# Kernel optimization log

Hardware: AMD Instinct MI355X
Metric: run time of the kernel (lower is better)

## Reference

```python
import jax, jax.numpy as jnp
import numpy as np
from jax import lax

B, S, E, H = 8, 1024, 1024, 16
HEAD_DIM = E // H
THRESHOLD = 0.5
NEG_FILL = -1e9


def setup_inputs() -> dict:
    key = jax.random.key(0)
    k0, k1, k2 = jax.random.split(key, 3)
    x = jax.random.normal(k0, (B, S, E), jnp.float32)
    in_proj_w = jax.random.normal(k1, (3 * E, E), jnp.float32) * 0.02
    in_proj_b = jnp.zeros((3 * E,), jnp.float32)
    out_proj_w = jax.random.normal(k2, (E, E), jnp.float32) * 0.02
    out_proj_b = jnp.zeros((E,), jnp.float32)
    return {"x": x, "in_proj_w": in_proj_w, "in_proj_b": in_proj_b,
            "out_proj_w": out_proj_w, "out_proj_b": out_proj_b}


def _mha(x, in_proj_w, in_proj_b, out_proj_w, out_proj_b):
    # PyTorch nn.MultiheadAttention with q=k=v=x, batch_first=True
    qkv = x @ in_proj_w.T + in_proj_b                     # [B,S,3E]
    q, k, v = jnp.split(qkv, 3, axis=-1)                  # each [B,S,E]
    def split_heads(t):
        return t.reshape(B, S, H, HEAD_DIM).transpose(0, 2, 1, 3)  # [B,H,S,d]
    q, k, v = split_heads(q), split_heads(k), split_heads(v)
    scale = 1.0 / np.sqrt(HEAD_DIM).astype(np.float32)
    scores = jnp.einsum('bhqd,bhkd->bhqk', q, k) * scale  # [B,H,S,S]
    w = jax.nn.softmax(scores, axis=-1)
    o = jnp.einsum('bhqk,bhkd->bhqd', w, v)               # [B,H,S,d]
    o = o.transpose(0, 2, 1, 3).reshape(B, S, E)
    attn_output = o @ out_proj_w.T + out_proj_b           # [B,S,E]
    attn_weights = w.mean(axis=1)                         # head-averaged [B,S,S]
    return attn_output, attn_weights


def _cluster(attn_weights):
    # Sequential greedy clustering: scan rows i in order; if row i is not yet
    # visited, its high-attention columns (> THRESHOLD) form cluster i and are
    # marked visited. cluster_id[b, j] = row index of the first cluster that
    # claimed token j, or -1 if never claimed.
    visited0 = jnp.zeros((B, S), dtype=bool)
    cid0 = jnp.full((B, S), -1, dtype=jnp.int32)

    def step(carry, i):
        visited, cid = carry
        process = ~jnp.take(visited, i, axis=1)           # [B] row i unvisited?
        high = jnp.take(attn_weights, i, axis=1) > THRESHOLD  # [B,S]
        claimed = process[:, None] & high                 # [B,S]
        newly = claimed & (~visited)
        cid = jnp.where(newly, jnp.int32(i), cid)
        visited = visited | claimed
        return (visited, cid), None

    (visited, cid), _ = lax.scan(step, (visited0, cid0), jnp.arange(S))
    return cid, visited


def reference(x, in_proj_w, in_proj_b, out_proj_w, out_proj_b):
    attn_output, attn_weights = _mha(x, in_proj_w, in_proj_b, out_proj_w, out_proj_b)
    cluster_ids, covered = _cluster(attn_weights)
    # _generate_image_features: x where token belongs to some cluster, -1e9 else
    clustered_outputs = jnp.where(covered[..., None], x, jnp.float32(NEG_FILL))
    return attn_output, attn_weights, clustered_outputs, cluster_ids
```

## Files before the change

### kernel.cpp

```cpp
#include <hip/hip_runtime.h>
#include <hip/hip_bf16.h>

#define B 8
#define S 1024
#define E 1024
#define H 16

typedef unsigned short u16;
typedef unsigned char u8;
typedef unsigned int u32;
typedef unsigned long long u64;

typedef __attribute__((ext_vector_type(8))) short s16x8;
typedef __attribute__((ext_vector_type(4))) float f32x4;
typedef __attribute__((ext_vector_type(16))) float f32x16;

__device__ __forceinline__ u16 f2bf(float f) {
    union { float f; u32 i; } x; x.f = f;
    u32 r = x.i + 0x7FFFu + ((x.i >> 16) & 1u);
    return (u16)(r >> 16);
}
__device__ __forceinline__ f32x16 zero16() {
    f32x16 z;
#pragma unroll
    for (int i = 0; i < 16; ++i) z[i] = 0.f;
    return z;
}
__device__ __forceinline__ void gload16(const u16* g, u16* l) {
    __builtin_amdgcn_global_load_lds(
        (const __attribute__((address_space(1))) u32*)g,
        (__attribute__((address_space(3))) u32*)l, 16, 0, 0);
}

__global__ __launch_bounds__(256) void cvt_all(
    const float* __restrict__ x, const float* __restrict__ w0,
    const float* __restrict__ w1, u16* __restrict__ xb,
    u16* __restrict__ wb0, u16* __restrict__ wb1) {
    int i = blockIdx.x * 256 + threadIdx.x;
    const float* src;
    u16* dst;
    int off;
    if (i < 2097152) { src = x; dst = xb; off = i; }
    else if (i < 2883584) { src = w0; dst = wb0; off = i - 2097152; }
    else { src = w1; dst = wb1; off = i - 2883584; }
    float4 v = ((const float4*)src)[off];
    union { u16 u[4]; ushort4 s; } p;
    p.u[0] = f2bf(v.x); p.u[1] = f2bf(v.y);
    p.u[2] = f2bf(v.z); p.u[3] = f2bf(v.w);
    ((ushort4*)dst)[off] = p.s;
}

__global__ __launch_bounds__(256) void gemm_qkv(
    const u16* __restrict__ A, const u16* __restrict__ W,
    const float* __restrict__ bias, u16* __restrict__ qb, u16* __restrict__ kb,
    u16* __restrict__ vt) {
    __shared__ __align__(16) u16 smem[16384];
    u16* As = smem;
    u16* Bs = smem + 8192;
    const int t = threadIdx.x;
    const int lane = t & 63;
    const int w = t >> 6;
    const int lin = (int)(blockIdx.y * gridDim.x + blockIdx.x);
    const int xcd = lin & 7;
    const int idx = lin >> 3;
    const int mt = (xcd & 3) * 16 + idx / 12;
    const int nt = (xcd >> 2) * 12 + idx % 12;
    const int m0 = mt * 128;
    const int n0 = nt * 128;
    const int wm = w >> 1, wn = w & 1;
    const int l15 = lane & 15, l4 = lane >> 4;
    const int lr = lane >> 3;
    const int lc = ((lane & 7) ^ lr) * 8;

    f32x4 acc[4][4];
#pragma unroll
    for (int i = 0; i < 4; ++i)
#pragma unroll
        for (int j = 0; j < 4; ++j) acc[i][j] = {0.f, 0.f, 0.f, 0.f};

    for (int k0 = 0; k0 < 1024; k0 += 64) {
        __syncthreads();
#pragma unroll
        for (int jj = 0; jj < 4; ++jj) {
            int j = w * 4 + jj;
            gload16(A + (size_t)(m0 + j * 8 + lr) * 1024 + k0 + lc, As + j * 512);
            gload16(W + (size_t)(n0 + j * 8 + lr) * 1024 + k0 + lc, Bs + j * 512);
        }
        __syncthreads();
#pragma unroll
        for (int ks = 0; ks < 2; ++ks) {
            s16x8 af[4], bf[4];
#pragma unroll
            for (int i = 0; i < 4; ++i) {
                int row = wm * 64 + i * 16 + l15;
                af[i] = *(const s16x8*)((const u8*)As +
                        (((row << 7) + (ks << 6) + (l4 << 4)) ^ ((row & 7) << 4)));
            }
#pragma unroll
            for (int j = 0; j < 4; ++j) {
                int row = wn * 64 + j * 16 + l15;
                bf[j] = *(const s16x8*)((const u8*)Bs +
                        (((row << 7) + (ks << 6) + (l4 << 4)) ^ ((row & 7) << 4)));
            }
#pragma unroll
            for (int i = 0; i < 4; ++i)
#pragma unroll
                for (int j = 0; j < 4; ++j)
                    acc[i][j] = __builtin_amdgcn_mfma_f32_16x16x32_bf16(
                        af[i], bf[j], acc[i][j], 0, 0, 0);
        }
    }

    __syncthreads();
    u16* Cs = smem;
    const int seg = n0 >> 10;
    const int bb = m0 >> 10;
    const int ms = m0 & 1023;
    if (seg < 2) {
        const float sc = (seg == 0) ? 0.18033688011f : 1.0f;
#pragma unroll
        for (int j = 0; j < 4; ++j) {
            int nl = wn * 64 + j * 16 + l15;
            float bn = bias[n0 + nl];
#pragma unroll
            for (int i = 0; i < 4; ++i) {
                int ml = wm * 64 + i * 16 + l4 * 4;
#pragma unroll
                for (int rr = 0; rr < 4; ++rr)
                    Cs[(ml + rr) * 128 + nl] = f2bf((acc[i][j][rr] + bn) * sc);
            }
        }
        __syncthreads();
        u16* dst0 = (seg == 0) ? qb : kb;
#pragma unroll
        for (int it = 0; it < 8; ++it) {
            int flat = it * 256 + t;
            int ml = flat >> 4;
            int g = (flat >> 3) & 1;
            int c8 = flat & 7;
            int hh = ((n0 + g * 64) & 1023) >> 6;
            u16* dst = dst0 + (((size_t)(bb * 16 + hh) * 1024 + ms + ml) << 6) + c8 * 8;
            *(uint4*)dst = *(const uint4*)(Cs + ml * 128 + g * 64 + c8 * 8);
        }
    } else {
#pragma unroll
        for (int j = 0; j < 4; ++j) {
            int nl = wn * 64 + j * 16 + l15;
            float bn = bias[n0 + nl];
            int sz = (nl & 7) << 4;
#pragma unroll
            for (int i = 0; i < 4; ++i) {
                int ml = wm * 64 + i * 16 + l4 * 4;
#pragma unroll
                for (int rr = 0; rr < 4; ++rr) {
                    int bl = (ml + rr) << 1;
                    *(u16*)((u8*)Cs + (nl << 8) + (bl ^ sz)) =
                        f2bf(acc[i][j][rr] + bn);
                }
            }
        }
        __syncthreads();
#pragma unroll
        for (int it = 0; it < 8; ++it) {
            int flat = it * 256 + t;
            int nl = flat >> 4;
            int c = flat & 15;
            int n = n0 + nl;
            int hh = (n & 1023) >> 6;
            int d = n & 63;
            u16* dst = vt + ((size_t)(bb * 16 + hh) * 64 + d) * 1024 + ms + c * 8;
            *(uint4*)dst = *(const uint4*)((u8*)Cs + (nl << 8) +
                                           ((c << 4) ^ ((nl & 7) << 4)));
        }
    }
}

__device__ __forceinline__ void gemm1_body(
    int lin, u16* smem, const u16* __restrict__ A, const u16* __restrict__ W,
    const float* __restrict__ bias, float* __restrict__ outf) {
    u16* As = smem;
    u16* Bs = smem + 8192;
    const int t = threadIdx.x;
    const int lane = t & 63;
    const int w = t >> 6;
    const int xcd = lin & 7;
    const int idx = lin >> 3;
    const int m0 = (xcd * 8 + idx / 8) * 128;
    const int n0 = (idx % 8) * 128;
    const int wm = w >> 1, wn = w & 1;
    const int l15 = lane & 15, l4 = lane >> 4;
    const int lr = lane >> 3;
    const int lc = ((lane & 7) ^ lr) * 8;

    f32x4 acc[4][4];
#pragma unroll
    for (int i = 0; i < 4; ++i)
#pragma unroll
        for (int j = 0; j < 4; ++j) acc[i][j] = {0.f, 0.f, 0.f, 0.f};

    for (int k0 = 0; k0 < 1024; k0 += 64) {
        __syncthreads();
#pragma unroll
        for (int jj = 0; jj < 4; ++jj) {
            int j = w * 4 + jj;
            gload16(A + (size_t)(m0 + j * 8 + lr) * 1024 + k0 + lc, As + j * 512);
            gload16(W + (size_t)(n0 + j * 8 + lr) * 1024 + k0 + lc, Bs + j * 512);
        }
        __syncthreads();
#pragma unroll
        for (int ks = 0; ks < 2; ++ks) {
            s16x8 af[4], bf[4];
#pragma unroll
            for (int i = 0; i < 4; ++i) {
                int row = wm * 64 + i * 16 + l15;
                af[i] = *(const s16x8*)((const u8*)As +
                        (((row << 7) + (ks << 6) + (l4 << 4)) ^ ((row & 7) << 4)));
            }
#pragma unroll
            for (int j = 0; j < 4; ++j) {
                int row = wn * 64 + j * 16 + l15;
                bf[j] = *(const s16x8*)((const u8*)Bs +
                        (((row << 7) + (ks << 6) + (l4 << 4)) ^ ((row & 7) << 4)));
            }
#pragma unroll
            for (int i = 0; i < 4; ++i)
#pragma unroll
                for (int j = 0; j < 4; ++j)
                    acc[i][j] = __builtin_amdgcn_mfma_f32_16x16x32_bf16(
                        af[i], bf[j], acc[i][j], 0, 0, 0);
        }
    }

    __syncthreads();
    float* Csf = (float*)smem;
#pragma unroll
    for (int r = 0; r < 2; ++r) {
        if (wm == r) {
#pragma unroll
            for (int j = 0; j < 4; ++j) {
                int nl = wn * 64 + j * 16 + l15;
                float bn = bias[n0 + nl];
#pragma unroll
                for (int i = 0; i < 4; ++i) {
                    int mlr = i * 16 + l4 * 4;
#pragma unroll
                    for (int rr = 0; rr < 4; ++rr)
                        Csf[(mlr + rr) * 128 + nl] = acc[i][j][rr] + bn;
                }
            }
        }
        __syncthreads();
#pragma unroll
        for (int it = 0; it < 8; ++it) {
            int flat = it * 256 + t;
            int row = flat >> 5;
            int c4 = flat & 31;
            *(float4*)(outf + (size_t)(m0 + r * 64 + row) * 1024 + n0 + c4 * 4) =
                *(const float4*)(Csf + row * 128 + c4 * 4);
        }
        __syncthreads();
    }
}

template <int BASE>
__device__ __forceinline__ s16x8 build_pa(f32x16 e) {
    u32 a, bv, c, d;
    asm("v_cvt_pk_bf16_f32 %0, %1, %2" : "=v"(a) : "v"(e[BASE + 0]), "v"(e[BASE + 1]));
    asm("v_cvt_pk_bf16_f32 %0, %1, %2" : "=v"(bv) : "v"(e[BASE + 2]), "v"(e[BASE + 3]));
    asm("v_cvt_pk_bf16_f32 %0, %1, %2" : "=v"(c) : "v"(e[BASE + 4]), "v"(e[BASE + 5]));
    asm("v_cvt_pk_bf16_f32 %0, %1, %2" : "=v"(d) : "v"(e[BASE + 6]), "v"(e[BASE + 7]));
    asm("v_permlane32_swap_b32 %0, %1" : "+v"(a), "+v"(c));
    asm("v_permlane32_swap_b32 %0, %1" : "+v"(bv), "+v"(d));
    union { u32 w[4]; s16x8 v; } u;
    u.w[0] = a; u.w[1] = bv; u.w[2] = c; u.w[3] = d;
    return u.v;
}
__device__ __forceinline__ float pair_sum(float v) {
    float a_ = v, b_ = v;
    asm("v_permlane32_swap_b32 %0, %1" : "+v"(a_), "+v"(b_));
    return a_ + b_;
}
__device__ __forceinline__ u32 pair_or(u32 v) {
    u32 a_ = v, b_ = v;
    asm("v_permlane32_swap_b32 %0, %1" : "+v"(a_), "+v"(b_));
    return a_ | b_;
}

__global__ __launch_bounds__(256, 3) void attn_flash(
    const u16* __restrict__ qg, const u16* __restrict__ kg,
    const u16* __restrict__ vtg, u16* __restrict__ og,
    float* __restrict__ stats) {
    __shared__ __align__(16) u16 bufK[2][64 * 64];
    __shared__ __align__(16) u16 bufV[2][64 * 64];
    const int t = threadIdx.x;
    const int lane = t & 63;
    const int w = t >> 6;
    const int task = ((blockIdx.x & 7) << 7) | (blockIdx.x >> 3);
    const int b = task >> 7;
    const int h = (task >> 3) & 15;
    const int qg_ = task & 7;
    const int q = lane & 31;
    const int hi = lane >> 5;
    const int q0 = qg_ * 128 + w * 32;
    const size_t hb = (size_t)(b * 16 + h) << 16;

    const int lr = lane >> 3;
    const int lc = ((lane & 7) ^ lr) * 8;
    const int swz = (q & 7) << 4;

#define STAGE(tt, bb)                                                          \
    do {                                                                       \
        _Pragma("unroll") for (int jj = 0; jj < 2; ++jj) {                     \
            int j = w * 2 + jj;                                                \
            gload16(kg + hb + (size_t)((tt) * 64 + j * 8 + lr) * 64 + lc,      \
                    bufK[bb] + j * 512);                                       \
            gload16(vtg + hb + (size_t)(j * 8 + lr) * 1024 + (tt) * 64 + lc,   \
                    bufV[bb] + j * 512);                                       \
        }                                                                      \
    } while (0)

    s16x8 qf[4];
#pragma unroll
    for (int s = 0; s < 4; ++s)
        qf[s] = *(const s16x8*)(qg + hb + (size_t)(q0 + q) * 64 + s * 16 + hi * 8);

    f32x16 oLo = zero16(), oHi = zero16();
    float l = 0.f;

    STAGE(0, 0);
    __syncthreads();
    int cur = 0;

    for (int tile = 0; tile < 16; ++tile) {
        if (tile < 15) STAGE(tile + 1, cur ^ 1);
        const u16* bK = bufK[cur];
        const u16* bV = bufV[cur];
        s16x8 ka0[4], ka1[4];
#pragma unroll
        for (int s = 0; s < 4; ++s) {
            ka0[s] = *(const s16x8*)((const u8*)bK +
                     (((q << 7) + (s << 5) + (hi << 4)) ^ swz));
            ka1[s] = *(const s16x8*)((const u8*)bK +
                     ((((32 + q) << 7) + (s << 5) + (hi << 4)) ^ swz));
        }
        f32x16 s0_ = zero16(), s1_ = zero16();
#pragma unroll
        for (int s = 0; s < 4; ++s) {
            s0_ = __builtin_amdgcn_mfma_f32_32x32x16_bf16(ka0[s], qf[s], s0_, 0, 0, 0);
            s1_ = __builtin_amdgcn_mfma_f32_32x32x16_bf16(ka1[s], qf[s], s1_, 0, 0, 0);
        }
        float t0 = 0.f, t1 = 0.f, t2 = 0.f, t3 = 0.f;
#pragma unroll
        for (int i = 0; i < 16; i += 4) {
            s0_[i + 0] = exp2f(s0_[i + 0]); s1_[i + 0] = exp2f(s1_[i + 0]);
            s0_[i + 1] = exp2f(s0_[i + 1]); s1_[i + 1] = exp2f(s1_[i + 1]);
            s0_[i + 2] = exp2f(s0_[i + 2]); s1_[i + 2] = exp2f(s1_[i + 2]);
            s0_[i + 3] = exp2f(s0_[i + 3]); s1_[i + 3] = exp2f(s1_[i + 3]);
            t0 += s0_[i + 0] + s1_[i + 0]; t1 += s0_[i + 1] + s1_[i + 1];
            t2 += s0_[i + 2] + s1_[i + 2]; t3 += s0_[i + 3] + s1_[i + 3];
        }
        l += pair_sum((t0 + t1) + (t2 + t3));
        s16x8 p00 = build_pa<0>(s0_), p01 = build_pa<8>(s0_);
        s16x8 p10 = build_pa<0>(s1_), p11 = build_pa<8>(s1_);
        s16x8 vA = *(const s16x8*)((const u8*)bV + (((q << 7) + 0 + (hi << 4)) ^ swz));
        s16x8 vB = *(const s16x8*)((const u8*)bV + ((((q + 32) << 7) + 0 + (hi << 4)) ^ swz));
        oLo = __builtin_amdgcn_mfma_f32_32x32x16_bf16(vA, p00, oLo, 0, 0, 0);
        oHi = __builtin_amdgcn_mfma_f32_32x32x16_bf16(vB, p00, oHi, 0, 0, 0);
        vA = *(const s16x8*)((const u8*)bV + (((q << 7) + 32 + (hi << 4)) ^ swz));
        vB = *(const s16x8*)((const u8*)bV + ((((q + 32) << 7) + 32 + (hi << 4)) ^ swz));
        oLo = __builtin_amdgcn_mfma_f32_32x32x16_bf16(vA, p01, oLo, 0, 0, 0);
        oHi = __builtin_amdgcn_mfma_f32_32x32x16_bf16(vB, p01, oHi, 0, 0, 0);
        vA = *(const s16x8*)((const u8*)bV + (((q << 7) + 64 + (hi << 4)) ^ swz));
        vB = *(const s16x8*)((const u8*)bV + ((((q + 32) << 7) + 64 + (hi << 4)) ^ swz));
        oLo = __builtin_amdgcn_mfma_f32_32x32x16_bf16(vA, p10, oLo, 0, 0, 0);
        oHi = __builtin_amdgcn_mfma_f32_32x32x16_bf16(vB, p10, oHi, 0, 0, 0);
        vA = *(const s16x8*)((const u8*)bV + (((q << 7) + 96 + (hi << 4)) ^ swz));
        vB = *(const s16x8*)((const u8*)bV + ((((q + 32) << 7) + 96 + (hi << 4)) ^ swz));
        oLo = __builtin_amdgcn_mfma_f32_32x32x16_bf16(vA, p11, oLo, 0, 0, 0);
        oHi = __builtin_amdgcn_mfma_f32_32x32x16_bf16(vB, p11, oHi, 0, 0, 0);
        __syncthreads();
        cur ^= 1;
    }
#undef STAGE
    float inv = 1.0f / l;
    oLo = oLo * inv;
    oHi = oHi * inv;
    u16* orow = og + (size_t)(b * 1024 + q0 + q) * 1024 + h * 64;
#pragma unroll
    for (int rg = 0; rg < 4; ++rg) {
        union { u16 u[4]; u64 v; } pk;
#pragma unroll
        for (int j = 0; j < 4; ++j) pk.u[j] = f2bf(oLo[4 * rg + j]);
        *(u64*)(orow + 8 * rg + 4 * hi) = pk.v;
#pragma unroll
        for (int j = 0; j < 4; ++j) pk.u[j] = f2bf(oHi[4 * rg + j]);
        *(u64*)(orow + 32 + 4 * hi + 8 * rg) = pk.v;
    }
    if (hi == 0)
        stats[(size_t)(b * 16 + h) * 1024 + q0 + q] = 4.0f + log2f(l);
}

__device__ __forceinline__ void aw_body(
    int bid, u16* smem, const u16* __restrict__ qg, const u16* __restrict__ kg,
    const float* __restrict__ stats, float* __restrict__ aw,
    u64* __restrict__ maskg) {
    u16* bufK = smem;
    u16* bufQ = smem + 8192;
    const int t = threadIdx.x;
    const int lane = t & 63;
    const int w = t >> 6;
    const int sw = ((bid & 7) << 7) | (bid >> 3);
    const int b = sw >> 7;
    const int ks = (sw >> 3) & 15;
    const int qg_ = sw & 7;
    const int q = lane & 31;
    const int hi = lane >> 5;
    const int q0 = qg_ * 128;
    const int qr = w * 32 + q;
    const int kbase = ks * 64;

    const int lr = lane >> 3;
    const int lc = ((lane & 7) ^ lr) * 8;
    const int swz = (q & 7) << 4;

#define STAGEAW(hh, bb)                                                        \
    do {                                                                       \
        const size_t hbs = (size_t)(b * 16 + (hh)) << 16;                      \
        _Pragma("unroll") for (int jj = 0; jj < 2; ++jj) {                     \
            int j = w * 2 + jj;                                                \
            gload16(kg + hbs + (size_t)(kbase + j * 8 + lr) * 64 + lc,         \
                    bufK + (bb) * 4096 + j * 512);                             \
        }                                                                      \
        _Pragma("unroll") for (int jj = 0; jj < 4; ++jj) {                     \
            int j = w * 4 + jj;                                                \
            gload16(qg + hbs + (size_t)(q0 + j * 8 + lr) * 64 + lc,            \
                    bufQ + (bb) * 8192 + j * 512);                             \
        }                                                                      \
    } while (0)

    f32x16 awA = zero16(), awB = zero16();

    STAGEAW(0, 0);
    __syncthreads();
    int cur = 0;

    for (int h = 0; h < 16; ++h) {
        if (h < 15) STAGEAW(h + 1, cur ^ 1);
        const u16* bK = bufK + cur * 4096;
        const u16* bQ = bufQ + cur * 8192;
        s16x8 qf[4], kA[4], kB[4];
#pragma unroll
        for (int s = 0; s < 4; ++s) {
            qf[s] = *(const s16x8*)((const u8*)bQ +
                    (((qr << 7) + (s << 5) + (hi << 4)) ^ swz));
            kA[s] = *(const s16x8*)((const u8*)bK +
                    (((q << 7) + (s << 5) + (hi << 4)) ^ swz));
            kB[s] = *(const s16x8*)((const u8*)bK +
                    ((((q + 32) << 7) + (s << 5) + (hi << 4)) ^ swz));
        }
        float C = stats[(size_t)(b * 16 + h) * 1024 + q0 + qr];
        f32x16 sA, sB;
        const float negC = -C;
#pragma unroll
        for (int i = 0; i < 16; ++i) { sA[i] = negC; sB[i] = negC; }
#pragma unroll
        for (int s = 0; s < 4; ++s) {
            sA = __builtin_amdgcn_mfma_f32_32x32x16_bf16(kA[s], qf[s], sA, 0, 0, 0);
            sB = __builtin_amdgcn_mfma_f32_32x32x16_bf16(kB[s], qf[s], sB, 0, 0, 0);
        }
#pragma unroll
        for (int i = 0; i < 16; ++i) {
            awA[i] += exp2f(sA[i]);
            awB[i] += exp2f(sB[i]);
        }
        __syncthreads();
        cur ^= 1;
    }
#undef STAGEAW
    float* awrow = aw + (size_t)(b * 1024 + q0 + qr) * 1024 + kbase;
#pragma unroll
    for (int rg = 0; rg < 4; ++rg) {
        *(float4*)(awrow + 8 * rg + 4 * hi) =
            make_float4(awA[4 * rg + 0], awA[4 * rg + 1], awA[4 * rg + 2], awA[4 * rg + 3]);
        *(float4*)(awrow + 32 + 8 * rg + 4 * hi) =
            make_float4(awB[4 * rg + 0], awB[4 * rg + 1], awB[4 * rg + 2], awB[4 * rg + 3]);
    }
    u32 lo = 0, hi32 = 0;
#pragma unroll
    for (int r = 0; r < 16; ++r) {
        int k = (r & 3) + 8 * (r >> 2) + 4 * hi;
        lo |= (awA[r] > 0.5f) ? (1u << k) : 0u;
        hi32 |= (awB[r] > 0.5f) ? (1u << k) : 0u;
    }
    lo = pair_or(lo);
    hi32 = pair_or(hi32);
    if (hi == 0)
        maskg[(size_t)(b * 1024 + q0 + qr) * 16 + ks] = ((u64)hi32 << 32) | (u64)lo;
}

__global__ __launch_bounds__(256, 3) void attn_aw_k(
    const u16* __restrict__ qg, const u16* __restrict__ kg,
    const float* __restrict__ stats, float* __restrict__ aw,
    u64* __restrict__ maskg) {
    __shared__ __align__(16) u16 sm[24576];
    aw_body((int)blockIdx.x, sm, qg, kg, stats, aw, maskg);
}
__global__ __launch_bounds__(256, 3) void gemm1_k(
    const u16* __restrict__ A, const u16* __restrict__ W,
    const float* __restrict__ bias, float* __restrict__ outf) {
    __shared__ __align__(16) u16 sm[16384];
    gemm1_body((int)blockIdx.x, sm, A, W, bias, outf);
}
__global__ __launch_bounds__(256, 3) void fused_aw_gemm1(
    const u16* __restrict__ qg, const u16* __restrict__ kg,
    const float* __restrict__ stats, float* __restrict__ aw,
    u64* __restrict__ maskg, const u16* __restrict__ o,
    const u16* __restrict__ w1, const float* __restrict__ bias,
    float* __restrict__ outf) {
    __shared__ __align__(16) u16 sm[24576];
    if (blockIdx.x < 1024)
        aw_body((int)blockIdx.x, sm, qg, kg, stats, aw, maskg);
    else
        gemm1_body((int)blockIdx.x - 1024, sm, o, w1, bias, outf);
}

__global__ __launch_bounds__(256) void cluster_kernel(
    const u64* __restrict__ maskg, float* __restrict__ cid, u64* __restrict__ cov) {
    __shared__ u64 mask[16384];
    __shared__ u16 rows[1024];
    const int t = threadIdx.x;
    const int b = blockIdx.x;
#pragma unroll
    for (int i = 0; i < 64; ++i)
        mask[t + 256 * i] = maskg[(size_t)b * 16384 + t + 256 * i];
#pragma unroll
    for (int i = 0; i < 4; ++i) cid[b * S + t + 256 * i] = -1.0f;
    __syncthreads();
    if (t < 64) {
        int nr = 0;
        for (int it = 0; it < 16; ++it) {
            int row = it * 64 + t;
            const u64* mp = mask + row * 16;
            u64 orv = 0;
#pragma unroll
            for (int j = 0; j < 16; ++j) orv |= mp[j];
            u64 bal = __ballot(orv != 0ULL);
            int pre = __popcll(bal & ((1ULL << t) - 1ULL));
            if (orv != 0ULL) rows[nr + pre] = (u16)row;
            nr += __popcll(bal);
        }
        u64 vis = 0;
        for (int idx = 0; idx < nr; ++idx) {
            int i = rows[idx];
            u64 viw = __shfl(vis, i >> 6);
            bool proc = ((viw >> (i & 63)) & 1ULL) == 0ULL;
            u64 cl = (proc && t < 16) ? mask[i * 16 + t] : 0ULL;
            u64 newly = cl & ~vis;
            vis |= cl;
            while (newly) {
                int bit = __ffsll((long long)newly) - 1;
                cid[b * S + t * 64 + bit] = (float)i;
                newly &= newly - 1;
            }
        }
        if (t < 16) cov[b * 16 + t] = vis;
    }
}

__global__ __launch_bounds__(256) void clustered_kernel(
    const float* __restrict__ x, const u64* __restrict__ cov,
    float* __restrict__ out2) {
    const size_t n4 = (size_t)B * S * E / 4;
    size_t idx = (size_t)blockIdx.x * 256 + threadIdx.x;
    const float4 neg = make_float4(-1e9f, -1e9f, -1e9f, -1e9f);
    for (; idx < n4; idx += (size_t)gridDim.x * 256) {
        size_t tok = idx >> 8;
        int bb = (int)(tok >> 10), s = (int)(tok & 1023);
        u64 m = cov[bb * 16 + (s >> 6)];
        bool c = ((m >> (s & 63)) & 1ULL) != 0ULL;
        float4 v = ((const float4*)x)[idx];
        ((float4*)out2)[idx] = c ? v : neg;
    }
}

extern "C" void kernel_launch(void* const* d_in, const int* in_sizes, int n_in,
                              void* d_out, int out_size, void* d_ws, size_t ws_size,
                              hipStream_t stream) {
    const float* x = (const float*)d_in[0];
    const float* w_in = (const float*)d_in[1];
    const float* b_in = (const float*)d_in[2];
    const float* w_out = (const float*)d_in[3];
    const float* b_out = (const float*)d_in[4];

    float* out0 = (float*)d_out;
    float* out1 = out0 + 8388608;
    float* out2 = out1 + 8388608;
    float* out3 = out2 + 8388608;

    if (ws_size >= ((size_t)37 << 20)) {
        u16* o_bf = (u16*)d_ws;
        u16* q_bf = (u16*)((char*)d_ws + ((size_t)16 << 20));
        u16* wb1 = (u16*)((char*)d_ws + ((size_t)32 << 20));
        float* statsF = (float*)((char*)d_ws + ((size_t)34 << 20));
        u64* maskg = (u64*)((char*)d_ws + ((size_t)34 << 20) + (1u << 19));
        u64* cov = (u64*)((char*)d_ws + ((size_t)35 << 20) + (1u << 19));
        u16* vt_bf = (u16*)out0;
        u16* xb = (u16*)out1;
        u16* wb0 = xb + 8388608;
        u16* k_bf = (u16*)out2;

        cvt_all<<<12288, 256, 0, stream>>>(x, w_in, w_out, xb, wb0, wb1);
        gemm_qkv<<<dim3(64, 24), 256, 0, stream>>>(xb, wb0, b_in, q_bf, k_bf, vt_bf);
        attn_flash<<<1024, 256, 0, stream>>>(q_bf, k_bf, vt_bf, o_bf, statsF);
        fused_aw_gemm1<<<1536, 256, 0, stream>>>(q_bf, k_bf, statsF, out1, maskg,
                                                 o_bf, wb1, b_out, out0);
        cluster_kernel<<<8, 256, 0, stream>>>(maskg, out3, cov);
        clustered_kernel<<<2048, 256, 0, stream>>>(x, cov, out2);
    } else {
        u16* q_bf = (u16*)out0;
        u16* vt_bf = q_bf + 8388608;
        u16* xb = (u16*)out1;
        u16* k_bf = (u16*)out2;
        u16* wb0 = k_bf + 8388608;
        u16* wb1 = wb0 + 3145728;
        float* statsF = (float*)(k_bf + 12582912);
        u16* o_bf = (u16*)d_ws;
        u64* maskg = (u64*)((char*)d_ws + (size_t)(16u << 20));
        u64* cov = (u64*)((char*)d_ws + (size_t)(17u << 20));

        cvt_all<<<12288, 256, 0, stream>>>(x, w_in, w_out, xb, wb0, wb1);
        gemm_qkv<<<dim3(64, 24), 256, 0, stream>>>(xb, wb0, b_in, q_bf, k_bf, vt_bf);
        attn_flash<<<1024, 256, 0, stream>>>(q_bf, k_bf, vt_bf, o_bf, statsF);
        attn_aw_k<<<1024, 256, 0, stream>>>(q_bf, k_bf, statsF, out1, maskg);
        gemm1_k<<<512, 256, 0, stream>>>(o_bf, wb1, b_out, out0);
        cluster_kernel<<<8, 256, 0, stream>>>(maskg, out3, cov);
        clustered_kernel<<<2048, 256, 0, stream>>>(x, cov, out2);
    }
}
```

Before: 222.2 us.

## Rewrite QKV GEMM with 256x256 tiles and a multi-stage async-load pipeline

Recasts the QKV projection GEMM as 512-thread blocks that each compute a 256x256 output tile from a 128KB shared buffer. K-tiles are prefetched two stages ahead in quadrant pieces, with vmcnt-based waits, raw barriers and setprio around the MFMA bursts. The goal is to overlap global loads with matrix math and to cut how often A and W are reloaded from memory. In exchange, shared memory per block and register pressure rise, and only 384 blocks are launched.

```diff
diff --git a/kernel.cpp b/kernel.cpp
--- a/kernel.cpp
+++ b/kernel.cpp
@@ -50,66 +50,97 @@
     ((ushort4*)dst)[off] = p.s;
 }
 
-__global__ __launch_bounds__(256) void gemm_qkv(
+__global__ __launch_bounds__(512, 2) void gemm_qkv(
     const u16* __restrict__ A, const u16* __restrict__ W,
     const float* __restrict__ bias, u16* __restrict__ qb, u16* __restrict__ kb,
     u16* __restrict__ vt) {
-    __shared__ __align__(16) u16 smem[16384];
-    u16* As = smem;
-    u16* Bs = smem + 8192;
+    __shared__ __align__(16) u16 smem[65536];
     const int t = threadIdx.x;
     const int lane = t & 63;
     const int w = t >> 6;
-    const int lin = (int)(blockIdx.y * gridDim.x + blockIdx.x);
+    const int lin = (int)blockIdx.x;
     const int xcd = lin & 7;
     const int idx = lin >> 3;
-    const int mt = (xcd & 3) * 16 + idx / 12;
-    const int nt = (xcd >> 2) * 12 + idx % 12;
-    const int m0 = mt * 128;
-    const int n0 = nt * 128;
-    const int wm = w >> 1, wn = w & 1;
+    const int mt = (xcd & 3) * 8 + idx / 6;
+    const int nt = (xcd >> 2) * 6 + idx % 6;
+    const int m0 = mt * 256;
+    const int n0 = nt * 256;
     const int l15 = lane & 15, l4 = lane >> 4;
     const int lr = lane >> 3;
     const int lc = ((lane & 7) ^ lr) * 8;
-
-    f32x4 acc[4][4];
-#pragma unroll
-    for (int i = 0; i < 4; ++i)
-#pragma unroll
-        for (int j = 0; j < 4; ++j) acc[i][j] = {0.f, 0.f, 0.f, 0.f};
-
-    for (int k0 = 0; k0 < 1024; k0 += 64) {
-        __syncthreads();
-#pragma unroll
-        for (int jj = 0; jj < 4; ++jj) {
-            int j = w * 4 + jj;
-            gload16(A + (size_t)(m0 + j * 8 + lr) * 1024 + k0 + lc, As + j * 512);
-            gload16(W + (size_t)(n0 + j * 8 + lr) * 1024 + k0 + lc, Bs + j * 512);
-        }
-        __syncthreads();
-#pragma unroll
-        for (int ks = 0; ks < 2; ++ks) {
-            s16x8 af[4], bf[4];
-#pragma unroll
-            for (int i = 0; i < 4; ++i) {
-                int row = wm * 64 + i * 16 + l15;
-                af[i] = *(const s16x8*)((const u8*)As +
-                        (((row << 7) + (ks << 6) + (l4 << 4)) ^ ((row & 7) << 4)));
-            }
-#pragma unroll
-            for (int j = 0; j < 4; ++j) {
-                int row = wn * 64 + j * 16 + l15;
-                bf[j] = *(const s16x8*)((const u8*)Bs +
-                        (((row << 7) + (ks << 6) + (l4 << 4)) ^ ((row & 7) << 4)));
-            }
-#pragma unroll
-            for (int i = 0; i < 4; ++i)
-#pragma unroll
-                for (int j = 0; j < 4; ++j)
-                    acc[i][j] = __builtin_amdgcn_mfma_f32_16x16x32_bf16(
-                        af[i], bf[j], acc[i][j], 0, 0, 0);
-        }
-    }
+    const int wmr = (w >> 2) * 64;
+    const int wnc = (w & 3) * 32;
+
+    f32x4 acc[4][4][2];
+#pragma unroll
+    for (int qd = 0; qd < 4; ++qd)
+#pragma unroll
+        for (int mi = 0; mi < 4; ++mi)
+#pragma unroll
+            for (int ni = 0; ni < 2; ++ni) acc[qd][mi][ni] = {0.f, 0.f, 0.f, 0.f};
+
+#define STG(KT, ISB, HH)                                                       \
+    do {                                                                       \
+        u16* dsth = smem + ((ISB) ? 32768 : 0) + (((KT) & 1) * 2 + (HH)) * 8192; \
+        const u16* srcb = (ISB) ? W : A;                                       \
+        int rbase = ((ISB) ? n0 : m0) + (HH) * 128;                            \
+        _Pragma("unroll") for (int jj = 0; jj < 2; ++jj) {                     \
+            int idx8 = w * 2 + jj;                                             \
+            gload16(srcb + (size_t)(rbase + idx8 * 8 + lr) * 1024 +            \
+                        (KT) * 64 + lc,                                        \
+                    dsth + idx8 * 512);                                        \
+        }                                                                      \
+    } while (0)
+
+#define PHASE(KT, MH, NH, SG, SKT, SISB, SHH, VMZ)                             \
+    do {                                                                       \
+        const u16* Ab = smem + (((KT) & 1) * 2 + (MH)) * 8192;                 \
+        const u16* Bb = smem + 32768 + (((KT) & 1) * 2 + (NH)) * 8192;         \
+        s16x8 af[4][2], bf[2][2];                                              \
+        _Pragma("unroll") for (int mi = 0; mi < 4; ++mi) {                     \
+            int r = wmr + mi * 16 + l15;                                       \
+            _Pragma("unroll") for (int ks = 0; ks < 2; ++ks)                   \
+                af[mi][ks] = *(const s16x8*)((const u8*)Ab +                   \
+                    (((r << 7) + (ks << 6) + (l4 << 4)) ^ ((r & 7) << 4)));    \
+        }                                                                      \
+        _Pragma("unroll") for (int ni = 0; ni < 2; ++ni) {                     \
+            int r = wnc + ni * 16 + l15;                                       \
+            _Pragma("unroll") for (int ks = 0; ks < 2; ++ks)                   \
+                bf[ni][ks] = *(const s16x8*)((const u8*)Bb +                   \
+                    (((r << 7) + (ks << 6) + (l4 << 4)) ^ ((r & 7) << 4)));    \
+        }                                                                      \
+        if (SG) STG(SKT, SISB, SHH);                                           \
+        if (VMZ) asm volatile("s_waitcnt vmcnt(0)" ::: "memory");              \
+        else     asm volatile("s_waitcnt vmcnt(6)" ::: "memory");              \
+        __builtin_amdgcn_s_barrier();                                          \
+        asm volatile("" ::: "memory");                                         \
+        __builtin_amdgcn_s_setprio(1);                                         \
+        _Pragma("unroll") for (int mi = 0; mi < 4; ++mi)                       \
+            _Pragma("unroll") for (int ni = 0; ni < 2; ++ni)                   \
+                _Pragma("unroll") for (int ks = 0; ks < 2; ++ks)               \
+                    acc[(MH)*2+(NH)][mi][ni] =                                 \
+                        __builtin_amdgcn_mfma_f32_16x16x32_bf16(               \
+                            af[mi][ks], bf[ni][ks], acc[(MH)*2+(NH)][mi][ni],  \
+                            0, 0, 0);                                          \
+        __builtin_amdgcn_s_setprio(0);                                         \
+    } while (0)
+
+    STG(0, 0, 0); STG(0, 1, 0); STG(0, 0, 1); STG(0, 1, 1);
+    STG(1, 0, 0); STG(1, 1, 0);
+    asm volatile("s_waitcnt vmcnt(6)" ::: "memory");
+    __builtin_amdgcn_s_barrier();
+    asm volatile("" ::: "memory");
+
+#pragma unroll 1
+    for (int kt = 0; kt < 16; ++kt) {
+        const int vz = (kt == 15);
+        PHASE(kt, 0, 0, (kt + 1 < 16), kt + 1, 0, 1, vz);
+        PHASE(kt, 0, 1, (kt + 1 < 16), kt + 1, 1, 1, vz);
+        PHASE(kt, 1, 0, (kt + 2 < 16), kt + 2, 0, 0, vz);
+        PHASE(kt, 1, 1, (kt + 2 < 16), kt + 2, 1, 0, vz);
+    }
+#undef PHASE
+#undef STG
 
     __syncthreads();
     u16* Cs = smem;
@@ -119,57 +150,69 @@
     if (seg < 2) {
         const float sc = (seg == 0) ? 0.18033688011f : 1.0f;
 #pragma unroll
-        for (int j = 0; j < 4; ++j) {
-            int nl = wn * 64 + j * 16 + l15;
-            float bn = bias[n0 + nl];
-#pragma unroll
-            for (int i = 0; i < 4; ++i) {
-                int ml = wm * 64 + i * 16 + l4 * 4;
-#pragma unroll
-                for (int rr = 0; rr < 4; ++rr)
-                    Cs[(ml + rr) * 128 + nl] = f2bf((acc[i][j][rr] + bn) * sc);
-            }
-        }
-        __syncthreads();
-        u16* dst0 = (seg == 0) ? qb : kb;
-#pragma unroll
-        for (int it = 0; it < 8; ++it) {
-            int flat = it * 256 + t;
-            int ml = flat >> 4;
-            int g = (flat >> 3) & 1;
-            int c8 = flat & 7;
-            int hh = ((n0 + g * 64) & 1023) >> 6;
-            u16* dst = dst0 + (((size_t)(bb * 16 + hh) * 1024 + ms + ml) << 6) + c8 * 8;
-            *(uint4*)dst = *(const uint4*)(Cs + ml * 128 + g * 64 + c8 * 8);
-        }
-    } else {
-#pragma unroll
-        for (int j = 0; j < 4; ++j) {
-            int nl = wn * 64 + j * 16 + l15;
-            float bn = bias[n0 + nl];
-            int sz = (nl & 7) << 4;
-#pragma unroll
-            for (int i = 0; i < 4; ++i) {
-                int ml = wm * 64 + i * 16 + l4 * 4;
-#pragma unroll
-                for (int rr = 0; rr < 4; ++rr) {
-                    int bl = (ml + rr) << 1;
-                    *(u16*)((u8*)Cs + (nl << 8) + (bl ^ sz)) =
-                        f2bf(acc[i][j][rr] + bn);
+        for (int qd = 0; qd < 4; ++qd) {
+            int rbase = (qd >> 1) * 128 + wmr;
+            int cbase = (qd & 1) * 128 + wnc;
+#pragma unroll
+            for (int ni = 0; ni < 2; ++ni) {
+                int col = cbase + ni * 16 + l15;
+                float bn = bias[n0 + col];
+#pragma unroll
+                for (int mi = 0; mi < 4; ++mi) {
+                    int row = rbase + mi * 16 + l4 * 4;
+#pragma unroll
+                    for (int rr = 0; rr < 4; ++rr)
+                        Cs[(row + rr) * 256 + col] =
+                            f2bf((acc[qd][mi][ni][rr] + bn) * sc);
                 }
             }
         }
         __syncthreads();
-#pragma unroll
-        for (int it = 0; it < 8; ++it) {
-            int flat = it * 256 + t;
-            int nl = flat >> 4;
-            int c = flat & 15;
+        u16* dst0 = (seg == 0) ? qb : kb;
+#pragma unroll
+        for (int it = 0; it < 16; ++it) {
+            int flat = it * 512 + t;
+            int ml = flat >> 5;
+            int c8 = flat & 31;
+            int n = n0 + c8 * 8;
+            int hh = (n & 1023) >> 6;
+            int d = n & 63;
+            u16* dst = dst0 + (((size_t)(bb * 16 + hh) * 1024 + ms + ml) << 6) + d;
+            *(uint4*)dst = *(const uint4*)(Cs + ml * 256 + c8 * 8);
+        }
+    } else {
+#pragma unroll
+        for (int qd = 0; qd < 4; ++qd) {
+            int rbase = (qd >> 1) * 128 + wmr;
+            int cbase = (qd & 1) * 128 + wnc;
+#pragma unroll
+            for (int ni = 0; ni < 2; ++ni) {
+                int nl = cbase + ni * 16 + l15;
+                float bn = bias[n0 + nl];
+                int sz = (nl & 7) << 4;
+#pragma unroll
+                for (int mi = 0; mi < 4; ++mi) {
+                    int ml = rbase + mi * 16 + l4 * 4;
+#pragma unroll
+                    for (int rr = 0; rr < 4; ++rr) {
+                        int bl = (ml + rr) << 1;
+                        *(u16*)((u8*)Cs + (nl << 9) + (bl ^ sz)) =
+                            f2bf(acc[qd][mi][ni][rr] + bn);
+                    }
+                }
+            }
+        }
+        __syncthreads();
+#pragma unroll
+        for (int it = 0; it < 16; ++it) {
+            int flat = it * 512 + t;
+            int nl = flat >> 5;
+            int c = flat & 31;
             int n = n0 + nl;
             int hh = (n & 1023) >> 6;
             int d = n & 63;
             u16* dst = vt + ((size_t)(bb * 16 + hh) * 64 + d) * 1024 + ms + c * 8;
-            *(uint4*)dst = *(const uint4*)((u8*)Cs + (nl << 8) +
+            *(uint4*)dst = *(const uint4*)((u8*)Cs + (nl << 9) +
                                            ((c << 4) ^ ((nl & 7) << 4)));
         }
     }
@@ -610,7 +653,7 @@
         u16* k_bf = (u16*)out2;
 
         cvt_all<<<12288, 256, 0, stream>>>(x, w_in, w_out, xb, wb0, wb1);
-        gemm_qkv<<<dim3(64, 24), 256, 0, stream>>>(xb, wb0, b_in, q_bf, k_bf, vt_bf);
+        gemm_qkv<<<384, 512, 0, stream>>>(xb, wb0, b_in, q_bf, k_bf, vt_bf);
         attn_flash<<<1024, 256, 0, stream>>>(q_bf, k_bf, vt_bf, o_bf, statsF);
         fused_aw_gemm1<<<1536, 256, 0, stream>>>(q_bf, k_bf, statsF, out1, maskg,
                                                  o_bf, wb1, b_out, out0);
@@ -629,7 +672,7 @@
         u64* cov = (u64*)((char*)d_ws + (size_t)(17u << 20));
 
         cvt_all<<<12288, 256, 0, stream>>>(x, w_in, w_out, xb, wb0, wb1);
-        gemm_qkv<<<dim3(64, 24), 256, 0, stream>>>(xb, wb0, b_in, q_bf, k_bf, vt_bf);
+        gemm_qkv<<<384, 512, 0, stream>>>(xb, wb0, b_in, q_bf, k_bf, vt_bf);
         attn_flash<<<1024, 256, 0, stream>>>(q_bf, k_bf, vt_bf, o_bf, statsF);
         attn_aw_k<<<1024, 256, 0, stream>>>(q_bf, k_bf, statsF, out1, maskg);
         gemm1_k<<<512, 256, 0, stream>>>(o_bf, wb1, b_out, out0);
```

Result: slower. 228.7 us (+2.9%).
